# Performance work log

Hardware: AMD Instinct MI355X
Metric: run time of the kernel (lower is better)

Reference implementation:

```python
import jax, jax.numpy as jnp
import numpy as np

NODES_PER_GRAPH = 116
HEADS = 2
D_HEAD = 116  # out_channels per head
HID = 256
B = 512
N = B * NODES_PER_GRAPH
DEG = 8
E = N * DEG
D_OUT = HEADS * D_HEAD  # 232


def setup_inputs() -> dict:
    key = jax.random.key(0)
    ks = jax.random.split(key, 6)
    h_flat = jax.random.normal(ks[0], (N, HID), dtype=jnp.float32)
    # every node receives DEG edges from random nodes within its own 116-node graph
    dst = jnp.repeat(jnp.arange(N, dtype=jnp.int64), DEG)
    offs = jax.random.randint(ks[1], (E,), 0, NODES_PER_GRAPH, dtype=jnp.int64)
    src = (dst // NODES_PER_GRAPH) * NODES_PER_GRAPH + offs
    edge_index = jnp.stack([src, dst], axis=0)
    batch_index = jnp.repeat(jnp.arange(B, dtype=jnp.int64), NODES_PER_GRAPH)
    s = 1.0 / np.sqrt(HID)
    Wq = jax.random.normal(ks[2], (HID, D_OUT), dtype=jnp.float32) * s
    Wk = jax.random.normal(ks[3], (HID, D_OUT), dtype=jnp.float32) * s
    Wv = jax.random.normal(ks[4], (HID, D_OUT), dtype=jnp.float32) * s
    Ws = jax.random.normal(ks[5], (HID, D_OUT), dtype=jnp.float32) * s
    return {"h_flat": h_flat, "edge_index": edge_index, "batch_index": batch_index,
            "Wq": Wq, "Wk": Wk, "Wv": Wv, "Ws": Ws}


def _graph_transformer_layer(h, edge_index, Wq, Wk, Wv, Ws):
    # PyG TransformerConv-style multi-head edge attention, concat heads + root skip.
    n = h.shape[0]
    q = (h @ Wq).reshape(n, HEADS, D_HEAD)
    k = (h @ Wk).reshape(n, HEADS, D_HEAD)
    v = (h @ Wv).reshape(n, HEADS, D_HEAD)
    src, dst = edge_index[0], edge_index[1]
    # per-edge scores [E, H]
    scores = jnp.einsum('ehd,ehd->eh', q[dst], k[src]) / np.sqrt(D_HEAD)
    # segment softmax over incoming edges of each dst node
    m = jax.ops.segment_max(scores, dst, num_segments=n)
    m = jnp.where(jnp.isfinite(m), m, 0.0)
    ex = jnp.exp(scores - m[dst])
    denom = jax.ops.segment_sum(ex, dst, num_segments=n)
    alpha_e = ex / (denom[dst] + 1e-16)
    msg = alpha_e[:, :, None] * v[src]                      # [E, H, Dh]
    attn = jax.ops.segment_sum(msg, dst, num_segments=n)    # [N, H, Dh]
    return attn.reshape(n, D_OUT) + h @ Ws


def reference(h_flat, edge_index, batch_index, Wq, Wk, Wv, Ws):
    n = h_flat.shape[0]
    b = n // NODES_PER_GRAPH
    h_proj = _graph_transformer_layer(h_flat, edge_index, Wq, Wk, Wv, Ws)  # [N, 232]
    e = h_proj.mean(axis=-1)                                 # [N]
    # scatter_softmax over per-graph node segments
    em = jax.ops.segment_max(e, batch_index, num_segments=b)
    ee = jnp.exp(e - em[batch_index])
    es = jax.ops.segment_sum(ee, batch_index, num_segments=b)
    alpha = ee / es[batch_index]                             # [N]
    h_weighted = alpha[:, None] * h_proj                     # [N, 232]
    alpha_map = alpha.reshape(b, NODES_PER_GRAPH)            # [B, 116]
    return alpha_map, h_weighted
```

## Files before the change

### kernel.cpp

```cpp
#include <hip/hip_runtime.h>

#define NODES  116
#define HEADS  2
#define DH     116
#define HID    256
#define NGRAPH 512
#define NN     (NGRAPH*NODES)
#define DEG    8
#define DOUT   (HEADS*DH)
#define RSTR   136

typedef short  s8v  __attribute__((ext_vector_type(8)));
typedef float  f4v  __attribute__((ext_vector_type(4)));

static __device__ __forceinline__ float bf2f(unsigned short u) {
    union { unsigned int i; float f; } c; c.i = ((unsigned int)u) << 16; return c.f;
}
static __device__ __forceinline__ unsigned short f2bf(float f) {
    union { float f; unsigned int u; } c; c.f = f;
    unsigned int u = c.u;
    unsigned int r = (u + 0x7FFFu + ((u >> 16) & 1u)) >> 16;
    return (unsigned short)r;
}

#define GLD_LDS16(gptr, lptr) \
    __builtin_amdgcn_global_load_lds((const __attribute__((address_space(1))) void*)(gptr), \
                                     (__attribute__((address_space(3))) void*)(lptr), 16, 0, 0)

__global__ __launch_bounds__(256) void prep_w(const float* __restrict__ Wq,
                                              const float* __restrict__ Wk,
                                              const float* __restrict__ Wv,
                                              const float* __restrict__ Ws,
                                              unsigned short* __restrict__ wt)
{
    unsigned int f = blockIdx.x * 256 + threadIdx.x;
    unsigned int n    = f & 127;
    unsigned int quad = (f >> 7) & 3;
    unsigned int kb   = (f >> 9) & 7;
    unsigned int ch   = (f >> 12) & 3;
    unsigned int hd   = f >> 14;
    unsigned short o[8] = {0,0,0,0,0,0,0,0};
    if (n < NODES) {
        unsigned int col = hd * DH + n;
        unsigned int k   = kb * 32 + quad * 8;
        const float* W = (ch == 0) ? Wq : (ch == 1) ? Wk : (ch == 2) ? Wv : Ws;
        #pragma unroll
        for (int i = 0; i < 8; i++)
            o[i] = f2bf(W[(size_t)(k + i) * DOUT + col]);
    }
    *(uint4*)(wt + (size_t)f * 8) = *(const uint4*)o;
}

__global__ __launch_bounds__(1024) void fused_gemm_attn(
    const float* __restrict__ h,
    const unsigned short* __restrict__ wt,
    const int* __restrict__ eidx,
    unsigned short* __restrict__ hp,
    float* __restrict__ psums)
{
    __shared__ unsigned short stA[4096];
    __shared__ unsigned short stB[4*4096];
    __shared__ unsigned short ql[128*RSTR];
    __shared__ unsigned short kl[128*RSTR];
    __shared__ unsigned short vt[128*RSTR];
    __shared__ int   srcl[NODES*DEG];
    __shared__ float scf[NODES*DEG];
    __shared__ float alph[NODES*DEG];

    const int b   = blockIdx.x;
    const int g   = b & 511;
    const int hd  = b >> 9;
    const int tid = threadIdx.x;
    const int w    = tid >> 6;
    const int lane = tid & 63;
    const int l15  = lane & 15;
    const int quad = lane >> 4;
    const int wm   = w >> 2;
    const int wn   = w & 3;

    if (tid < NODES * DEG)
        srcl[tid] = eidx[(size_t)g * NODES * DEG + tid] - g * NODES;

    const int am  = tid >> 3;
    const int q8  = tid & 7;
    long grow = (long)g * NODES + am;
    if (grow >= NN) grow = NN - 1;
    const float* hrow = h + (size_t)grow * HID + q8 * 4;
    unsigned short* aw = stA + ((q8 >> 1) * 128 + am) * 8 + (q8 & 1) * 4;

    f4v accq[2][2], acck[2][2], accv[2][2], accs[2][2];
    #pragma unroll
    for (int i = 0; i < 2; i++)
        #pragma unroll
        for (int j = 0; j < 2; j++)
            #pragma unroll
            for (int r = 0; r < 4; r++) {
                accq[i][j][r] = 0.f; acck[i][j][r] = 0.f;
                accv[i][j][r] = 0.f; accs[i][j][r] = 0.f;
            }

    const size_t wbase = (size_t)hd * 4 * 8 * 4096;

    for (int kb = 0; kb < 8; kb++) {
        float4 av = *(const float4*)(hrow + kb * 32);
        unsigned short o[4] = { f2bf(av.x), f2bf(av.y), f2bf(av.z), f2bf(av.w) };
        *(uint2*)aw = *(const uint2*)o;
        #pragma unroll
        for (int j = 0; j < 2; j++) {
            int c = w * 2 + j;
            int ch = c >> 3, sub = c & 7;
            const unsigned short* src = wt + wbase + ((size_t)(ch * 8 + kb)) * 4096 + sub * 512;
            GLD_LDS16((const char*)src + lane * 16, (char*)stB + c * 1024);
        }
        __syncthreads();

        s8v a0 = *(const s8v*)(stA + (quad * 128 + wm * 32 + l15) * 8);
        s8v a1 = *(const s8v*)(stA + (quad * 128 + wm * 32 + 16 + l15) * 8);
        #pragma unroll
        for (int ch = 0; ch < 4; ch++) {
            s8v b0 = *(const s8v*)(stB + ch * 4096 + (quad * 128 + wn * 32 + l15) * 8);
            s8v b1 = *(const s8v*)(stB + ch * 4096 + (quad * 128 + wn * 32 + 16 + l15) * 8);
            f4v (*acc)[2] = (ch == 0) ? accq : (ch == 1) ? acck : (ch == 2) ? accv : accs;
            acc[0][0] = __builtin_amdgcn_mfma_f32_16x16x32_bf16(a0, b0, acc[0][0], 0, 0, 0);
            acc[0][1] = __builtin_amdgcn_mfma_f32_16x16x32_bf16(a0, b1, acc[0][1], 0, 0, 0);
            acc[1][0] = __builtin_amdgcn_mfma_f32_16x16x32_bf16(a1, b0, acc[1][0], 0, 0, 0);
            acc[1][1] = __builtin_amdgcn_mfma_f32_16x16x32_bf16(a1, b1, acc[1][1], 0, 0, 0);
        }
        __syncthreads();
    }

    #pragma unroll
    for (int i = 0; i < 2; i++) {
        #pragma unroll
        for (int j = 0; j < 2; j++) {
            int col = wn * 32 + j * 16 + l15;
            #pragma unroll
            for (int r = 0; r < 4; r++) {
                int row = wm * 32 + i * 16 + quad * 4 + r;
                ql[row * RSTR + col] = (col < NODES) ? f2bf(accq[i][j][r]) : 0;
                kl[row * RSTR + col] = (col < NODES) ? f2bf(acck[i][j][r]) : 0;
                vt[col * RSTR + row] = (row < NODES) ? f2bf(accv[i][j][r]) : 0;
            }
        }
    }
    __syncthreads();

    f4v sacc[2][2];
    #pragma unroll
    for (int i = 0; i < 2; i++)
        #pragma unroll
        for (int j = 0; j < 2; j++)
            #pragma unroll
            for (int r = 0; r < 4; r++) sacc[i][j][r] = 0.f;
    #pragma unroll
    for (int ks = 0; ks < 4; ks++) {
        s8v a0 = *(const s8v*)(ql + (wm * 32 + l15) * RSTR + ks * 32 + quad * 8);
        s8v a1 = *(const s8v*)(ql + (wm * 32 + 16 + l15) * RSTR + ks * 32 + quad * 8);
        s8v b0 = *(const s8v*)(kl + (wn * 32 + l15) * RSTR + ks * 32 + quad * 8);
        s8v b1 = *(const s8v*)(kl + (wn * 32 + 16 + l15) * RSTR + ks * 32 + quad * 8);
        sacc[0][0] = __builtin_amdgcn_mfma_f32_16x16x32_bf16(a0, b0, sacc[0][0], 0, 0, 0);
        sacc[0][1] = __builtin_amdgcn_mfma_f32_16x16x32_bf16(a0, b1, sacc[0][1], 0, 0, 0);
        sacc[1][0] = __builtin_amdgcn_mfma_f32_16x16x32_bf16(a1, b0, sacc[1][0], 0, 0, 0);
        sacc[1][1] = __builtin_amdgcn_mfma_f32_16x16x32_bf16(a1, b1, sacc[1][1], 0, 0, 0);
    }
    #pragma unroll
    for (int i = 0; i < 2; i++) {
        #pragma unroll
        for (int r = 0; r < 4; r++) {
            int row = wm * 32 + i * 16 + quad * 4 + r;
            if (row < NODES) {
                #pragma unroll
                for (int j = 0; j < 2; j++) {
                    int col = wn * 32 + j * 16 + l15;
                    #pragma unroll
                    for (int e = 0; e < DEG; e++)
                        if (srcl[row * DEG + e] == col)
                            scf[row * DEG + e] = sacc[i][j][r];
                }
            }
        }
    }
    __syncthreads();

    if (tid < NODES * DEG) {
        float s = scf[tid] * 0.09284766908852594f;
        float m = s;
        m = fmaxf(m, __shfl_xor(m, 1));
        m = fmaxf(m, __shfl_xor(m, 2));
        m = fmaxf(m, __shfl_xor(m, 4));
        float e = __expf(s - m);
        float sum = e;
        sum += __shfl_xor(sum, 1);
        sum += __shfl_xor(sum, 2);
        sum += __shfl_xor(sum, 4);
        alph[tid] = e / sum;
    }
    for (int f = tid; f < 128 * RSTR / 4; f += 1024)
        *(uint2*)(kl + f * 4) = make_uint2(0u, 0u);
    __syncthreads();

    if (tid < NODES) {
        #pragma unroll
        for (int j = 0; j < DEG; j++) {
            int sj = srcl[tid * DEG + j];
            bool first = true;
            for (int jj = 0; jj < j; jj++) first = first && (srcl[tid * DEG + jj] != sj);
            if (first) {
                float a = alph[tid * DEG + j];
                for (int jj = j + 1; jj < DEG; jj++)
                    if (srcl[tid * DEG + jj] == sj) a += alph[tid * DEG + jj];
                kl[tid * RSTR + sj] = f2bf(a);
            }
        }
    }
    __syncthreads();

    #pragma unroll
    for (int ks = 0; ks < 4; ks++) {
        s8v a0 = *(const s8v*)(kl + (wm * 32 + l15) * RSTR + ks * 32 + quad * 8);
        s8v a1 = *(const s8v*)(kl + (wm * 32 + 16 + l15) * RSTR + ks * 32 + quad * 8);
        s8v b0 = *(const s8v*)(vt + (wn * 32 + l15) * RSTR + ks * 32 + quad * 8);
        s8v b1 = *(const s8v*)(vt + (wn * 32 + 16 + l15) * RSTR + ks * 32 + quad * 8);
        accs[0][0] = __builtin_amdgcn_mfma_f32_16x16x32_bf16(a0, b0, accs[0][0], 0, 0, 0);
        accs[0][1] = __builtin_amdgcn_mfma_f32_16x16x32_bf16(a0, b1, accs[0][1], 0, 0, 0);
        accs[1][0] = __builtin_amdgcn_mfma_f32_16x16x32_bf16(a1, b0, accs[1][0], 0, 0, 0);
        accs[1][1] = __builtin_amdgcn_mfma_f32_16x16x32_bf16(a1, b1, accs[1][1], 0, 0, 0);
    }
    __syncthreads();

    unsigned short* hpl = vt;
    #pragma unroll
    for (int i = 0; i < 2; i++) {
        #pragma unroll
        for (int j = 0; j < 2; j++) {
            int col = wn * 32 + j * 16 + l15;
            #pragma unroll
            for (int r = 0; r < 4; r++) {
                int row = wm * 32 + i * 16 + quad * 4 + r;
                hpl[row * RSTR + col] = f2bf(accs[i][j][r]);
            }
        }
    }
    __syncthreads();

    if (tid < NODES * DEG) {
        const int i  = tid >> 3;
        const int seg = tid & 7;
        float rs = 0.0f;
        #pragma unroll
        for (int t = 0; t < 2; t++) {
            int gi = seg + t * 8;
            if (gi < 15) {
                const s8v v8 = *(const s8v*)(hpl + i * RSTR + gi * 8);
                #pragma unroll
                for (int e = 0; e < 8; e++) rs += bf2f(((unsigned short*)&v8)[e]);
            }
        }
        rs += __shfl_xor(rs, 1);
        rs += __shfl_xor(rs, 2);
        rs += __shfl_xor(rs, 4);
        if (seg == 0) psums[((size_t)hd * NGRAPH + g) * NODES + i] = rs;
    }
    for (int f = tid; f < NODES * 29; f += 1024) {
        int r  = f / 29;
        int gi = f - r * 29;
        *(uint2*)(hp + ((size_t)(g * NODES + r)) * DOUT + hd * DH + gi * 4) =
            *(const uint2*)(hpl + r * RSTR + gi * 4);
    }
}

__global__ __launch_bounds__(256) void pool_k2(const unsigned short* __restrict__ hp,
                                               const float* __restrict__ psums,
                                               float* __restrict__ out_alpha,
                                               float* __restrict__ out_hw)
{
    __shared__ float ew[NODES];
    __shared__ float alph[NODES];
    __shared__ float red[2];

    const int g   = blockIdx.x;
    const int tid = threadIdx.x;

    if (tid < NODES)
        ew[tid] = (psums[(size_t)g * NODES + tid] +
                   psums[((size_t)NGRAPH + g) * NODES + tid]) * (1.0f / DOUT);
    __syncthreads();
    if (tid < 64) {
        float a = ew[tid];
        float b = (tid + 64 < NODES) ? ew[tid + 64] : -1e30f;
        float mm = fmaxf(a, b);
        #pragma unroll
        for (int off = 32; off > 0; off >>= 1) mm = fmaxf(mm, __shfl_down(mm, off));
        if (tid == 0) red[0] = mm;
    }
    __syncthreads();
    if (tid < NODES) ew[tid] = __expf(ew[tid] - red[0]);
    __syncthreads();
    if (tid < 64) {
        float a = ew[tid] + ((tid + 64 < NODES) ? ew[tid + 64] : 0.0f);
        #pragma unroll
        for (int off = 32; off > 0; off >>= 1) a += __shfl_down(a, off);
        if (tid == 0) red[1] = a;
    }
    __syncthreads();
    if (tid < NODES) {
        float al = ew[tid] / red[1];
        alph[tid] = al;
        out_alpha[(size_t)g * NODES + tid] = al;
    }
    __syncthreads();

    for (int f = tid; f < NODES * 58; f += 256) {
        int r  = f / 58;
        int gi = f - r * 58;
        float al = alph[r];
        uint2 hv = *(const uint2*)(hp + ((size_t)(g * NODES + r)) * DOUT + gi * 4);
        float4 o = make_float4(al * bf2f((unsigned short)(hv.x & 0xFFFF)),
                               al * bf2f((unsigned short)(hv.x >> 16)),
                               al * bf2f((unsigned short)(hv.y & 0xFFFF)),
                               al * bf2f((unsigned short)(hv.y >> 16)));
        *(float4*)(out_hw + ((size_t)(g * NODES + r)) * DOUT + gi * 4) = o;
    }
}

extern "C" void kernel_launch(void* const* d_in, const int* in_sizes, int n_in,
                              void* d_out, int out_size, void* d_ws, size_t ws_size,
                              hipStream_t stream)
{
    const float* h    = (const float*)d_in[0];
    const int*   eidx = (const int*)d_in[1];
    const float* Wq   = (const float*)d_in[3];
    const float* Wk   = (const float*)d_in[4];
    const float* Wv   = (const float*)d_in[5];
    const float* Ws   = (const float*)d_in[6];

    unsigned short* wt = (unsigned short*)d_ws;
    unsigned short* hp = wt + (size_t)262144;
    float*       psums = (float*)(hp + (size_t)13778944);

    float* out_alpha = (float*)d_out;
    float* out_hw    = out_alpha + NN;

    prep_w<<<128, 256, 0, stream>>>(Wq, Wk, Wv, Ws, wt);
    fused_gemm_attn<<<1024, 1024, 0, stream>>>(h, wt, eidx, hp, psums);
    pool_k2<<<NGRAPH, 256, 0, stream>>>(hp, psums, out_alpha, out_hw);
}
```

Baseline: 217.5 us.

## Fuse both heads and graph pooling into one per-graph kernel with double-buffered K loop

Each block now handles one graph and loops over both heads, then performs the per-graph softmax pooling and writes alpha and weighted outputs directly, removing the separate pool kernel and the psums round trip. Head 1's projection stays in shared memory while head 0 goes to a workspace and is reread. The GEMM K loop gets double-buffered A and B shared tiles so the next tile's loads overlap the MFMAs. The trade-off is half as many blocks (512 of 1024 threads) and more shared memory per block, which lowers parallelism and occupancy.

```diff
diff --git a/kernel.cpp b/kernel.cpp
--- a/kernel.cpp
+++ b/kernel.cpp
@@ -51,25 +51,24 @@
     *(uint4*)(wt + (size_t)f * 8) = *(const uint4*)o;
 }
 
-__global__ __launch_bounds__(1024) void fused_gemm_attn(
+__global__ __launch_bounds__(1024) void fused_all(
     const float* __restrict__ h,
     const unsigned short* __restrict__ wt,
     const int* __restrict__ eidx,
     unsigned short* __restrict__ hp,
-    float* __restrict__ psums)
+    float* __restrict__ out_alpha,
+    float* __restrict__ out_hw)
 {
-    __shared__ unsigned short stA[4096];
-    __shared__ unsigned short stB[4*4096];
-    __shared__ unsigned short ql[128*RSTR];
-    __shared__ unsigned short kl[128*RSTR];
-    __shared__ unsigned short vt[128*RSTR];
+    __shared__ __align__(16) unsigned short stA[2*4096];
+    __shared__ __align__(16) unsigned short stB[2*16384];
+    __shared__ __align__(16) unsigned short ql[128*RSTR];
+    __shared__ __align__(16) unsigned short kl[128*RSTR];
     __shared__ int   srcl[NODES*DEG];
     __shared__ float scf[NODES*DEG];
-    __shared__ float alph[NODES*DEG];
-
-    const int b   = blockIdx.x;
-    const int g   = b & 511;
-    const int hd  = b >> 9;
+    __shared__ float ps[2][NODES];
+    __shared__ float red[2];
+
+    const int g   = blockIdx.x;
     const int tid = threadIdx.x;
     const int w    = tid >> 6;
     const int lane = tid & 63;
@@ -81,245 +80,275 @@
     if (tid < NODES * DEG)
         srcl[tid] = eidx[(size_t)g * NODES * DEG + tid] - g * NODES;
 
-    const int am  = tid >> 3;
-    const int q8  = tid & 7;
+    const int am = tid >> 3;
+    const int q8 = tid & 7;
     long grow = (long)g * NODES + am;
     if (grow >= NN) grow = NN - 1;
     const float* hrow = h + (size_t)grow * HID + q8 * 4;
-    unsigned short* aw = stA + ((q8 >> 1) * 128 + am) * 8 + (q8 & 1) * 4;
-
-    f4v accq[2][2], acck[2][2], accv[2][2], accs[2][2];
-    #pragma unroll
-    for (int i = 0; i < 2; i++)
-        #pragma unroll
-        for (int j = 0; j < 2; j++)
-            #pragma unroll
-            for (int r = 0; r < 4; r++) {
-                accq[i][j][r] = 0.f; acck[i][j][r] = 0.f;
-                accv[i][j][r] = 0.f; accs[i][j][r] = 0.f;
-            }
-
-    const size_t wbase = (size_t)hd * 4 * 8 * 4096;
-
-    for (int kb = 0; kb < 8; kb++) {
-        float4 av = *(const float4*)(hrow + kb * 32);
-        unsigned short o[4] = { f2bf(av.x), f2bf(av.y), f2bf(av.z), f2bf(av.w) };
-        *(uint2*)aw = *(const uint2*)o;
-        #pragma unroll
-        for (int j = 0; j < 2; j++) {
-            int c = w * 2 + j;
-            int ch = c >> 3, sub = c & 7;
-            const unsigned short* src = wt + wbase + ((size_t)(ch * 8 + kb)) * 4096 + sub * 512;
-            GLD_LDS16((const char*)src + lane * 16, (char*)stB + c * 1024);
-        }
-        __syncthreads();
-
-        s8v a0 = *(const s8v*)(stA + (quad * 128 + wm * 32 + l15) * 8);
-        s8v a1 = *(const s8v*)(stA + (quad * 128 + wm * 32 + 16 + l15) * 8);
-        #pragma unroll
-        for (int ch = 0; ch < 4; ch++) {
-            s8v b0 = *(const s8v*)(stB + ch * 4096 + (quad * 128 + wn * 32 + l15) * 8);
-            s8v b1 = *(const s8v*)(stB + ch * 4096 + (quad * 128 + wn * 32 + 16 + l15) * 8);
-            f4v (*acc)[2] = (ch == 0) ? accq : (ch == 1) ? acck : (ch == 2) ? accv : accs;
-            acc[0][0] = __builtin_amdgcn_mfma_f32_16x16x32_bf16(a0, b0, acc[0][0], 0, 0, 0);
-            acc[0][1] = __builtin_amdgcn_mfma_f32_16x16x32_bf16(a0, b1, acc[0][1], 0, 0, 0);
-            acc[1][0] = __builtin_amdgcn_mfma_f32_16x16x32_bf16(a1, b0, acc[1][0], 0, 0, 0);
-            acc[1][1] = __builtin_amdgcn_mfma_f32_16x16x32_bf16(a1, b1, acc[1][1], 0, 0, 0);
-        }
-        __syncthreads();
-    }
-
-    #pragma unroll
-    for (int i = 0; i < 2; i++) {
-        #pragma unroll
-        for (int j = 0; j < 2; j++) {
-            int col = wn * 32 + j * 16 + l15;
+    const int aoff = ((q8 >> 1) * 128 + am) * 8 + (q8 & 1) * 4;
+
+    for (int hd = 0; hd < 2; hd++) {
+        const size_t wbase = (size_t)hd * 4 * 8 * 4096;
+
+        f4v accq[2][2], acck[2][2], accv[2][2], accs[2][2];
+        #pragma unroll
+        for (int i = 0; i < 2; i++)
+            #pragma unroll
+            for (int j = 0; j < 2; j++)
+                #pragma unroll
+                for (int r = 0; r < 4; r++) {
+                    accq[i][j][r] = 0.f; acck[i][j][r] = 0.f;
+                    accv[i][j][r] = 0.f; accs[i][j][r] = 0.f;
+                }
+
+        {
+            float4 av = *(const float4*)(hrow);
+            #pragma unroll
+            for (int j = 0; j < 2; j++) {
+                int c = w * 2 + j;
+                int ch = c >> 3, sub = c & 7;
+                const unsigned short* src = wt + wbase + ((size_t)(ch * 8 + 0)) * 4096 + sub * 512;
+                GLD_LDS16((const char*)src + lane * 16, (char*)stB + c * 1024);
+            }
+            unsigned short o[4] = { f2bf(av.x), f2bf(av.y), f2bf(av.z), f2bf(av.w) };
+            *(uint2*)(stA + aoff) = *(const uint2*)o;
+        }
+        __syncthreads();
+
+        int cur = 0;
+        for (int kb = 0; kb < 8; kb++) {
+            float4 av;
+            if (kb < 7) {
+                av = *(const float4*)(hrow + (kb + 1) * 32);
+                #pragma unroll
+                for (int j = 0; j < 2; j++) {
+                    int c = w * 2 + j;
+                    int ch = c >> 3, sub = c & 7;
+                    const unsigned short* src = wt + wbase + ((size_t)(ch * 8 + kb + 1)) * 4096 + sub * 512;
+                    GLD_LDS16((const char*)src + lane * 16,
+                              (char*)stB + (cur ^ 1) * 32768 + c * 1024);
+                }
+            }
+            const unsigned short* sa = stA + cur * 4096;
+            const unsigned short* sb = stB + cur * 16384;
+            s8v a0 = *(const s8v*)(sa + (quad * 128 + wm * 32 + l15) * 8);
+            s8v a1 = *(const s8v*)(sa + (quad * 128 + wm * 32 + 16 + l15) * 8);
+            #pragma unroll
+            for (int ch = 0; ch < 4; ch++) {
+                s8v b0 = *(const s8v*)(sb + ch * 4096 + (quad * 128 + wn * 32 + l15) * 8);
+                s8v b1 = *(const s8v*)(sb + ch * 4096 + (quad * 128 + wn * 32 + 16 + l15) * 8);
+                f4v (*acc)[2] = (ch == 0) ? accq : (ch == 1) ? acck : (ch == 2) ? accv : accs;
+                acc[0][0] = __builtin_amdgcn_mfma_f32_16x16x32_bf16(a0, b0, acc[0][0], 0, 0, 0);
+                acc[0][1] = __builtin_amdgcn_mfma_f32_16x16x32_bf16(a0, b1, acc[0][1], 0, 0, 0);
+                acc[1][0] = __builtin_amdgcn_mfma_f32_16x16x32_bf16(a1, b0, acc[1][0], 0, 0, 0);
+                acc[1][1] = __builtin_amdgcn_mfma_f32_16x16x32_bf16(a1, b1, acc[1][1], 0, 0, 0);
+            }
+            if (kb < 7) {
+                unsigned short o[4] = { f2bf(av.x), f2bf(av.y), f2bf(av.z), f2bf(av.w) };
+                *(uint2*)(stA + (cur ^ 1) * 4096 + aoff) = *(const uint2*)o;
+            }
+            __syncthreads();
+            cur ^= 1;
+        }
+
+        #pragma unroll
+        for (int i = 0; i < 2; i++) {
+            #pragma unroll
+            for (int j = 0; j < 2; j++) {
+                int col = wn * 32 + j * 16 + l15;
+                #pragma unroll
+                for (int r = 0; r < 4; r++) {
+                    int row = wm * 32 + i * 16 + quad * 4 + r;
+                    ql[row * RSTR + col] = (col < NODES) ? f2bf(accq[i][j][r]) : 0;
+                    kl[row * RSTR + col] = (col < NODES) ? f2bf(acck[i][j][r]) : 0;
+                }
+            }
+        }
+        __syncthreads();
+
+        f4v sacc[2][2];
+        #pragma unroll
+        for (int i = 0; i < 2; i++)
+            #pragma unroll
+            for (int j = 0; j < 2; j++)
+                #pragma unroll
+                for (int r = 0; r < 4; r++) sacc[i][j][r] = 0.f;
+        #pragma unroll
+        for (int ks = 0; ks < 4; ks++) {
+            s8v a0 = *(const s8v*)(ql + (wm * 32 + l15) * RSTR + ks * 32 + quad * 8);
+            s8v a1 = *(const s8v*)(ql + (wm * 32 + 16 + l15) * RSTR + ks * 32 + quad * 8);
+            s8v b0 = *(const s8v*)(kl + (wn * 32 + l15) * RSTR + ks * 32 + quad * 8);
+            s8v b1 = *(const s8v*)(kl + (wn * 32 + 16 + l15) * RSTR + ks * 32 + quad * 8);
+            sacc[0][0] = __builtin_amdgcn_mfma_f32_16x16x32_bf16(a0, b0, sacc[0][0], 0, 0, 0);
+            sacc[0][1] = __builtin_amdgcn_mfma_f32_16x16x32_bf16(a0, b1, sacc[0][1], 0, 0, 0);
+            sacc[1][0] = __builtin_amdgcn_mfma_f32_16x16x32_bf16(a1, b0, sacc[1][0], 0, 0, 0);
+            sacc[1][1] = __builtin_amdgcn_mfma_f32_16x16x32_bf16(a1, b1, sacc[1][1], 0, 0, 0);
+        }
+        #pragma unroll
+        for (int i = 0; i < 2; i++) {
             #pragma unroll
             for (int r = 0; r < 4; r++) {
                 int row = wm * 32 + i * 16 + quad * 4 + r;
-                ql[row * RSTR + col] = (col < NODES) ? f2bf(accq[i][j][r]) : 0;
-                kl[row * RSTR + col] = (col < NODES) ? f2bf(acck[i][j][r]) : 0;
-                vt[col * RSTR + row] = (row < NODES) ? f2bf(accv[i][j][r]) : 0;
-            }
-        }
-    }
-    __syncthreads();
-
-    f4v sacc[2][2];
-    #pragma unroll
-    for (int i = 0; i < 2; i++)
-        #pragma unroll
-        for (int j = 0; j < 2; j++)
-            #pragma unroll
-            for (int r = 0; r < 4; r++) sacc[i][j][r] = 0.f;
-    #pragma unroll
-    for (int ks = 0; ks < 4; ks++) {
-        s8v a0 = *(const s8v*)(ql + (wm * 32 + l15) * RSTR + ks * 32 + quad * 8);
-        s8v a1 = *(const s8v*)(ql + (wm * 32 + 16 + l15) * RSTR + ks * 32 + quad * 8);
-        s8v b0 = *(const s8v*)(kl + (wn * 32 + l15) * RSTR + ks * 32 + quad * 8);
-        s8v b1 = *(const s8v*)(kl + (wn * 32 + 16 + l15) * RSTR + ks * 32 + quad * 8);
-        sacc[0][0] = __builtin_amdgcn_mfma_f32_16x16x32_bf16(a0, b0, sacc[0][0], 0, 0, 0);
-        sacc[0][1] = __builtin_amdgcn_mfma_f32_16x16x32_bf16(a0, b1, sacc[0][1], 0, 0, 0);
-        sacc[1][0] = __builtin_amdgcn_mfma_f32_16x16x32_bf16(a1, b0, sacc[1][0], 0, 0, 0);
-        sacc[1][1] = __builtin_amdgcn_mfma_f32_16x16x32_bf16(a1, b1, sacc[1][1], 0, 0, 0);
-    }
-    #pragma unroll
-    for (int i = 0; i < 2; i++) {
-        #pragma unroll
-        for (int r = 0; r < 4; r++) {
-            int row = wm * 32 + i * 16 + quad * 4 + r;
-            if (row < NODES) {
-                #pragma unroll
-                for (int j = 0; j < 2; j++) {
-                    int col = wn * 32 + j * 16 + l15;
+                if (row < NODES) {
                     #pragma unroll
-                    for (int e = 0; e < DEG; e++)
-                        if (srcl[row * DEG + e] == col)
-                            scf[row * DEG + e] = sacc[i][j][r];
-                }
-            }
-        }
-    }
-    __syncthreads();
-
-    if (tid < NODES * DEG) {
-        float s = scf[tid] * 0.09284766908852594f;
-        float m = s;
-        m = fmaxf(m, __shfl_xor(m, 1));
-        m = fmaxf(m, __shfl_xor(m, 2));
-        m = fmaxf(m, __shfl_xor(m, 4));
-        float e = __expf(s - m);
-        float sum = e;
-        sum += __shfl_xor(sum, 1);
-        sum += __shfl_xor(sum, 2);
-        sum += __shfl_xor(sum, 4);
-        alph[tid] = e / sum;
-    }
-    for (int f = tid; f < 128 * RSTR / 4; f += 1024)
-        *(uint2*)(kl + f * 4) = make_uint2(0u, 0u);
-    __syncthreads();
-
-    if (tid < NODES) {
-        #pragma unroll
-        for (int j = 0; j < DEG; j++) {
-            int sj = srcl[tid * DEG + j];
-            bool first = true;
-            for (int jj = 0; jj < j; jj++) first = first && (srcl[tid * DEG + jj] != sj);
-            if (first) {
-                float a = alph[tid * DEG + j];
-                for (int jj = j + 1; jj < DEG; jj++)
-                    if (srcl[tid * DEG + jj] == sj) a += alph[tid * DEG + jj];
-                kl[tid * RSTR + sj] = f2bf(a);
-            }
-        }
-    }
-    __syncthreads();
-
-    #pragma unroll
-    for (int ks = 0; ks < 4; ks++) {
-        s8v a0 = *(const s8v*)(kl + (wm * 32 + l15) * RSTR + ks * 32 + quad * 8);
-        s8v a1 = *(const s8v*)(kl + (wm * 32 + 16 + l15) * RSTR + ks * 32 + quad * 8);
-        s8v b0 = *(const s8v*)(vt + (wn * 32 + l15) * RSTR + ks * 32 + quad * 8);
-        s8v b1 = *(const s8v*)(vt + (wn * 32 + 16 + l15) * RSTR + ks * 32 + quad * 8);
-        accs[0][0] = __builtin_amdgcn_mfma_f32_16x16x32_bf16(a0, b0, accs[0][0], 0, 0, 0);
-        accs[0][1] = __builtin_amdgcn_mfma_f32_16x16x32_bf16(a0, b1, accs[0][1], 0, 0, 0);
-        accs[1][0] = __builtin_amdgcn_mfma_f32_16x16x32_bf16(a1, b0, accs[1][0], 0, 0, 0);
-        accs[1][1] = __builtin_amdgcn_mfma_f32_16x16x32_bf16(a1, b1, accs[1][1], 0, 0, 0);
-    }
-    __syncthreads();
-
-    unsigned short* hpl = vt;
-    #pragma unroll
-    for (int i = 0; i < 2; i++) {
-        #pragma unroll
-        for (int j = 0; j < 2; j++) {
-            int col = wn * 32 + j * 16 + l15;
-            #pragma unroll
-            for (int r = 0; r < 4; r++) {
-                int row = wm * 32 + i * 16 + quad * 4 + r;
-                hpl[row * RSTR + col] = f2bf(accs[i][j][r]);
-            }
-        }
-    }
-    __syncthreads();
-
-    if (tid < NODES * DEG) {
-        const int i  = tid >> 3;
-        const int seg = tid & 7;
-        float rs = 0.0f;
-        #pragma unroll
-        for (int t = 0; t < 2; t++) {
-            int gi = seg + t * 8;
-            if (gi < 15) {
-                const s8v v8 = *(const s8v*)(hpl + i * RSTR + gi * 8);
-                #pragma unroll
-                for (int e = 0; e < 8; e++) rs += bf2f(((unsigned short*)&v8)[e]);
-            }
-        }
-        rs += __shfl_xor(rs, 1);
-        rs += __shfl_xor(rs, 2);
-        rs += __shfl_xor(rs, 4);
-        if (seg == 0) psums[((size_t)hd * NGRAPH + g) * NODES + i] = rs;
-    }
-    for (int f = tid; f < NODES * 29; f += 1024) {
-        int r  = f / 29;
-        int gi = f - r * 29;
-        *(uint2*)(hp + ((size_t)(g * NODES + r)) * DOUT + hd * DH + gi * 4) =
-            *(const uint2*)(hpl + r * RSTR + gi * 4);
-    }
-}
-
-__global__ __launch_bounds__(256) void pool_k2(const unsigned short* __restrict__ hp,
-                                               const float* __restrict__ psums,
-                                               float* __restrict__ out_alpha,
-                                               float* __restrict__ out_hw)
-{
-    __shared__ float ew[NODES];
-    __shared__ float alph[NODES];
-    __shared__ float red[2];
-
-    const int g   = blockIdx.x;
-    const int tid = threadIdx.x;
-
-    if (tid < NODES)
-        ew[tid] = (psums[(size_t)g * NODES + tid] +
-                   psums[((size_t)NGRAPH + g) * NODES + tid]) * (1.0f / DOUT);
+                    for (int j = 0; j < 2; j++) {
+                        int col = wn * 32 + j * 16 + l15;
+                        #pragma unroll
+                        for (int e = 0; e < DEG; e++)
+                            if (srcl[row * DEG + e] == col)
+                                scf[row * DEG + e] = sacc[i][j][r];
+                    }
+                }
+            }
+        }
+        __syncthreads();
+
+        for (int f = tid; f < 128 * RSTR / 8; f += 1024)
+            *(uint4*)(kl + (size_t)f * 8) = make_uint4(0u, 0u, 0u, 0u);
+        #pragma unroll
+        for (int i = 0; i < 2; i++) {
+            #pragma unroll
+            for (int j = 0; j < 2; j++) {
+                int col = wn * 32 + j * 16 + l15;
+                #pragma unroll
+                for (int r = 0; r < 4; r++) {
+                    int row = wm * 32 + i * 16 + quad * 4 + r;
+                    ql[col * RSTR + row] = (row < NODES) ? f2bf(accv[i][j][r]) : 0;
+                }
+            }
+        }
+        __syncthreads();
+
+        if (tid < NODES * DEG) {
+            float s = scf[tid] * 0.09284766908852594f;
+            float m = s;
+            m = fmaxf(m, __shfl_xor(m, 1));
+            m = fmaxf(m, __shfl_xor(m, 2));
+            m = fmaxf(m, __shfl_xor(m, 4));
+            float e = __expf(s - m);
+            float sum = e;
+            sum += __shfl_xor(sum, 1);
+            sum += __shfl_xor(sum, 2);
+            sum += __shfl_xor(sum, 4);
+            scf[tid] = e / sum;
+        }
+        __syncthreads();
+
+        if (tid < NODES) {
+            #pragma unroll
+            for (int j = 0; j < DEG; j++) {
+                int sj = srcl[tid * DEG + j];
+                bool first = true;
+                for (int jj = 0; jj < j; jj++) first = first && (srcl[tid * DEG + jj] != sj);
+                if (first) {
+                    float a = scf[tid * DEG + j];
+                    for (int jj = j + 1; jj < DEG; jj++)
+                        if (srcl[tid * DEG + jj] == sj) a += scf[tid * DEG + jj];
+                    kl[tid * RSTR + sj] = f2bf(a);
+                }
+            }
+        }
+        __syncthreads();
+
+        #pragma unroll
+        for (int ks = 0; ks < 4; ks++) {
+            s8v a0 = *(const s8v*)(kl + (wm * 32 + l15) * RSTR + ks * 32 + quad * 8);
+            s8v a1 = *(const s8v*)(kl + (wm * 32 + 16 + l15) * RSTR + ks * 32 + quad * 8);
+            s8v b0 = *(const s8v*)(ql + (wn * 32 + l15) * RSTR + ks * 32 + quad * 8);
+            s8v b1 = *(const s8v*)(ql + (wn * 32 + 16 + l15) * RSTR + ks * 32 + quad * 8);
+            accs[0][0] = __builtin_amdgcn_mfma_f32_16x16x32_bf16(a0, b0, accs[0][0], 0, 0, 0);
+            accs[0][1] = __builtin_amdgcn_mfma_f32_16x16x32_bf16(a0, b1, accs[0][1], 0, 0, 0);
+            accs[1][0] = __builtin_amdgcn_mfma_f32_16x16x32_bf16(a1, b0, accs[1][0], 0, 0, 0);
+            accs[1][1] = __builtin_amdgcn_mfma_f32_16x16x32_bf16(a1, b1, accs[1][1], 0, 0, 0);
+        }
+        __syncthreads();
+
+        #pragma unroll
+        for (int i = 0; i < 2; i++) {
+            #pragma unroll
+            for (int j = 0; j < 2; j++) {
+                int col = wn * 32 + j * 16 + l15;
+                #pragma unroll
+                for (int r = 0; r < 4; r++) {
+                    int row = wm * 32 + i * 16 + quad * 4 + r;
+                    ql[row * RSTR + col] = f2bf(accs[i][j][r]);
+                }
+            }
+        }
+        __syncthreads();
+
+        if (tid < NODES * DEG) {
+            const int i   = tid >> 3;
+            const int seg = tid & 7;
+            float rs = 0.0f;
+            #pragma unroll
+            for (int t = 0; t < 2; t++) {
+                int gi = seg + t * 8;
+                if (gi < 15) {
+                    const s8v v8 = *(const s8v*)(ql + i * RSTR + gi * 8);
+                    #pragma unroll
+                    for (int e = 0; e < 8; e++) rs += bf2f((unsigned short)v8[e]);
+                }
+            }
+            rs += __shfl_xor(rs, 1);
+            rs += __shfl_xor(rs, 2);
+            rs += __shfl_xor(rs, 4);
+            if (seg == 0) ps[hd][i] = rs;
+        }
+        if (hd == 0) {
+            for (int f = tid; f < NODES * 29; f += 1024) {
+                int r  = f / 29;
+                int gi = f - r * 29;
+                *(uint2*)(hp + ((size_t)g * NODES + r) * 116 + gi * 4) =
+                    *(const uint2*)(ql + r * RSTR + gi * 4);
+            }
+        }
+        __syncthreads();
+    }
+
+    if (tid < NODES) scf[tid] = (ps[0][tid] + ps[1][tid]) * (1.0f / DOUT);
     __syncthreads();
     if (tid < 64) {
-        float a = ew[tid];
-        float b = (tid + 64 < NODES) ? ew[tid + 64] : -1e30f;
+        float a = scf[tid];
+        float b = (tid + 64 < NODES) ? scf[tid + 64] : -1e30f;
         float mm = fmaxf(a, b);
         #pragma unroll
         for (int off = 32; off > 0; off >>= 1) mm = fmaxf(mm, __shfl_down(mm, off));
         if (tid == 0) red[0] = mm;
     }
     __syncthreads();
-    if (tid < NODES) ew[tid] = __expf(ew[tid] - red[0]);
+    if (tid < NODES) scf[tid] = __expf(scf[tid] - red[0]);
     __syncthreads();
     if (tid < 64) {
-        float a = ew[tid] + ((tid + 64 < NODES) ? ew[tid + 64] : 0.0f);
+        float a = scf[tid] + ((tid + 64 < NODES) ? scf[tid + 64] : 0.0f);
         #pragma unroll
         for (int off = 32; off > 0; off >>= 1) a += __shfl_down(a, off);
         if (tid == 0) red[1] = a;
     }
     __syncthreads();
     if (tid < NODES) {
-        float al = ew[tid] / red[1];
-        alph[tid] = al;
+        float al = scf[tid] / red[1];
+        scf[tid] = al;
         out_alpha[(size_t)g * NODES + tid] = al;
     }
     __syncthreads();
-
-    for (int f = tid; f < NODES * 58; f += 256) {
+    for (int f = tid; f < NODES * 58; f += 1024) {
         int r  = f / 58;
         int gi = f - r * 58;
-        float al = alph[r];
-        uint2 hv = *(const uint2*)(hp + ((size_t)(g * NODES + r)) * DOUT + gi * 4);
-        float4 o = make_float4(al * bf2f((unsigned short)(hv.x & 0xFFFF)),
-                               al * bf2f((unsigned short)(hv.x >> 16)),
-                               al * bf2f((unsigned short)(hv.y & 0xFFFF)),
-                               al * bf2f((unsigned short)(hv.y >> 16)));
-        *(float4*)(out_hw + ((size_t)(g * NODES + r)) * DOUT + gi * 4) = o;
+        float al = scf[r];
+        float4 o;
+        if (gi < 29) {
+            uint2 hv = *(const uint2*)(hp + ((size_t)g * NODES + r) * 116 + gi * 4);
+            o = make_float4(al * bf2f((unsigned short)(hv.x & 0xFFFF)),
+                            al * bf2f((unsigned short)(hv.x >> 16)),
+                            al * bf2f((unsigned short)(hv.y & 0xFFFF)),
+                            al * bf2f((unsigned short)(hv.y >> 16)));
+        } else {
+            const unsigned short* hv = ql + r * RSTR + (gi - 29) * 4;
+            o = make_float4(al * bf2f(hv[0]), al * bf2f(hv[1]),
+                            al * bf2f(hv[2]), al * bf2f(hv[3]));
+        }
+        *(float4*)(out_hw + ((size_t)g * NODES + r) * DOUT + gi * 4) = o;
     }
 }
 
@@ -336,12 +365,10 @@
 
     unsigned short* wt = (unsigned short*)d_ws;
     unsigned short* hp = wt + (size_t)262144;
-    float*       psums = (float*)(hp + (size_t)13778944);
 
     float* out_alpha = (float*)d_out;
     float* out_hw    = out_alpha + NN;
 
     prep_w<<<128, 256, 0, stream>>>(Wq, Wk, Wv, Ws, wt);
-    fused_gemm_attn<<<1024, 1024, 0, stream>>>(h, wt, eidx, hp, psums);
-    pool_k2<<<NGRAPH, 256, 0, stream>>>(hp, psums, out_alpha, out_hw);
-}
+    fused_all<<<NGRAPH, 1024, 0, stream>>>(h, wt, eidx, hp, out_alpha, out_hw);
+}
```

Result: slower. 246.9 us (+13.6%).
